# Performance work log

Measured on AMD Instinct MI355X. Metric: run time of the kernel, lower is better.

## Reference

```python
import jax, jax.numpy as jnp
import numpy as np

N_NODES = 50000
N_EDGES = 1_600_000
D_IN = 512
D_OUT = 512


def setup_inputs() -> dict:
    key = jax.random.key(0)
    k_x, k_w, k_b, k_r, k_c, k_e = jax.random.split(key, 6)
    x = jax.random.normal(k_x, (N_NODES, D_IN), dtype=jnp.float32)
    stdv = 1.0 / np.sqrt(D_OUT)
    weight = jax.random.uniform(k_w, (D_IN, D_OUT), minval=-stdv, maxval=stdv, dtype=jnp.float32)
    bias = jax.random.uniform(k_b, (D_OUT,), minval=-stdv, maxval=stdv, dtype=jnp.float32)
    row = jax.random.randint(k_r, (N_EDGES,), 0, N_NODES, dtype=jnp.int32)
    col = jax.random.randint(k_c, (N_EDGES,), 0, N_NODES, dtype=jnp.int32)
    edge_weight = jax.random.uniform(k_e, (N_EDGES,), dtype=jnp.float32)
    return {"x": x, "weight": weight, "bias": bias, "row": row, "col": col, "edge_weight": edge_weight}


def reference(x, weight, bias, row, col, edge_weight):
    # support = X @ W   [N, D_OUT]
    support = x @ weight
    # spmm: out[i] = sum_{e: row[e]==i} edge_weight[e] * support[col[e]]
    msgs = edge_weight[:, None] * support[col]  # [E, D_OUT]
    out = jax.ops.segment_sum(msgs, row, num_segments=N_NODES)
    return out + bias
```

## Files before the change

### kernel.cpp

```cpp
#include <hip/hip_runtime.h>
#include <hip/hip_fp16.h>

#define D_DIM 512
#define BM 128
#define BN 256
#define BK 64

typedef _Float16 h8 __attribute__((ext_vector_type(8)));
typedef _Float16 h4 __attribute__((ext_vector_type(4)));
typedef float f32x4 __attribute__((ext_vector_type(4)));
typedef unsigned int u32x4 __attribute__((ext_vector_type(4)));

#define LDS_PTR(p) ((__attribute__((address_space(3))) void*)(p))
#define GLB_PTR(p) ((const __attribute__((address_space(1))) void*)(p))


__global__ void k_count(const int* __restrict__ row, int* __restrict__ counts, int E) {
    int e = blockIdx.x * blockDim.x + threadIdx.x;
    if (e < E) atomicAdd(&counts[row[e]], 1);
}

__global__ void k_scan_part(const int* __restrict__ counts, int* __restrict__ offsets,
                            int* __restrict__ bsum, int n) {
    __shared__ int s[1024];
    int t = threadIdx.x;
    int i = blockIdx.x * 1024 + t;
    int v = (i < n) ? counts[i] : 0;
    s[t] = v;
    __syncthreads();
    for (int off = 1; off < 1024; off <<= 1) {
        int x = (t >= off) ? s[t - off] : 0;
        __syncthreads();
        s[t] += x;
        __syncthreads();
    }
    if (i < n) offsets[i] = s[t] - v;
    if (t == 1023) bsum[blockIdx.x] = s[t];
}

__global__ void k_scan_top(int* __restrict__ bsum, int* __restrict__ offsets, int nb, int n) {
    int t = threadIdx.x;
    int v = (t < nb) ? bsum[t] : 0;
    int orig = v;
    for (int off = 1; off < 64; off <<= 1) {
        int u = __shfl_up(v, off, 64);
        if (t >= off) v += u;
    }
    if (t < nb) bsum[t] = v - orig;
    if (t == nb - 1) offsets[n] = v;
}

__global__ void k_scan_add(int* __restrict__ offsets, int* __restrict__ cursor,
                           const int* __restrict__ bsum, int n) {
    int i = blockIdx.x * 1024 + threadIdx.x;
    if (i < n) {
        int o = offsets[i] + bsum[blockIdx.x];
        offsets[i] = o;
        cursor[i] = o;
    }
}

__global__ void k_scatter(const int* __restrict__ row, const int* __restrict__ col,
                          const float* __restrict__ ew, int* __restrict__ cursor,
                          uint2* __restrict__ packed, int E) {
    int e = blockIdx.x * blockDim.x + threadIdx.x;
    if (e < E) {
        int r = row[e];
        int pos = atomicAdd(&cursor[r], 1);
        packed[pos] = make_uint2((unsigned)col[e], __float_as_uint(ew[e]));
    }
}


__global__ void k_wt(const float* __restrict__ w, _Float16* __restrict__ wt) {
    __shared__ _Float16 tile[32][33];
    int bx = blockIdx.x & 15, by = blockIdx.x >> 4;
    int tx = threadIdx.x & 31, ty = threadIdx.x >> 5;
    for (int r = 0; r < 32; r += 8)
        tile[ty + r][tx] = (_Float16)w[(size_t)(by * 32 + ty + r) * 512 + bx * 32 + tx];
    __syncthreads();
    for (int r = 0; r < 32; r += 8)
        wt[(size_t)(bx * 32 + ty + r) * 512 + by * 32 + tx] = tile[tx][ty + r];
}


__launch_bounds__(256)
__global__ void k_gemm(const float* __restrict__ x, const _Float16* __restrict__ wt,
                       _Float16* __restrict__ sup, int M, int nwg) {
    __shared__ __align__(16) unsigned char As[BM * BK * 2];
    __shared__ __align__(16) unsigned char Bs[BN * BK * 2];

    const int orig = blockIdx.x;
    const int q = nwg >> 3, r = nwg & 7;
    const int xcd = orig & 7, idx = orig >> 3;
    const int wgid = (xcd < r ? xcd * (q + 1) : r * (q + 1) + (xcd - r) * q) + idx;
    const int m0 = (wgid >> 1) * BM, n0 = (wgid & 1) * BN;

    const int t = threadIdx.x;
    const int lane = t & 63, w = t >> 6;

    f32x4 acc[8][4] = {};

    const int ar_t = t >> 4;
    const int ac_t = (t & 15) * 4;
    const int bn_t = t >> 3;
    const int bk_sw = ((t & 7) * 16) ^ (((t >> 3) & 7) << 4);

    for (int kt = 0; kt < D_DIM / BK; ++kt) {
        const int k0 = kt * BK;
        for (int j = 0; j < 8; ++j) {
            int n = j * 32 + bn_t;
            const char* src = (const char*)(wt + (size_t)(n0 + n) * 512 + k0) + bk_sw;
            __builtin_amdgcn_global_load_lds(GLB_PTR(src), LDS_PTR(Bs + j * 4096 + t * 16),
                                             16, 0, 0);
        }
        for (int i = 0; i < 8; ++i) {
            int rr = i * 16 + ar_t;
            int g = m0 + rr;
            if (g >= M) g = M - 1;
            const float4 v = *(const float4*)(x + (size_t)g * 512 + k0 + ac_t);
            h4 hv;
            hv[0] = (_Float16)v.x; hv[1] = (_Float16)v.y;
            hv[2] = (_Float16)v.z; hv[3] = (_Float16)v.w;
            int addr = rr * 128 + ((ac_t * 2) ^ ((rr & 7) << 4));
            *(h4*)(As + addr) = hv;
        }
        __syncthreads();

        for (int ks = 0; ks < 2; ++ks) {
            h8 af[8], bf[4];
            const int kb = ks * 64 + ((lane >> 4) * 16);
#pragma unroll
            for (int mb = 0; mb < 8; ++mb) {
                int rr = mb * 16 + (lane & 15);
                af[mb] = *(const h8*)(As + rr * 128 + (kb ^ ((rr & 7) << 4)));
            }
#pragma unroll
            for (int nb = 0; nb < 4; ++nb) {
                int n = w * 64 + nb * 16 + (lane & 15);
                bf[nb] = *(const h8*)(Bs + n * 128 + (kb ^ ((n & 7) << 4)));
            }
#pragma unroll
            for (int mb = 0; mb < 8; ++mb)
#pragma unroll
                for (int nb = 0; nb < 4; ++nb)
                    acc[mb][nb] = __builtin_amdgcn_mfma_f32_16x16x32_f16(
                        af[mb], bf[nb], acc[mb][nb], 0, 0, 0);
        }
        __syncthreads();
    }

    const int cr = (lane >> 4) * 4, cc = lane & 15;
#pragma unroll
    for (int mb = 0; mb < 8; ++mb) {
#pragma unroll
        for (int nb = 0; nb < 4; ++nb) {
            int gn = n0 + w * 64 + nb * 16 + cc;
#pragma unroll
            for (int qq = 0; qq < 4; ++qq) {
                int gm = m0 + mb * 16 + cr + qq;
                if (gm < M)
                    sup[(size_t)gm * 512 + gn] = (_Float16)acc[mb][nb][qq];
            }
        }
    }
}


__global__ void k_spmm(const _Float16* __restrict__ sup, const uint2* __restrict__ packed,
                       const int* __restrict__ offsets, const float* __restrict__ bias,
                       float* __restrict__ out, int M) {
    const int i = blockIdx.x * 4 + (threadIdx.x >> 6);
    if (i >= M) return;
    const int l = threadIdx.x & 63;
    const int s0 = offsets[i], s1 = offsets[i + 1];
    const _Float16* __restrict__ supl = sup + l * 8;

    float acc[8];
    {
        const float4 b0 = *(const float4*)(bias + l * 8);
        const float4 b1 = *(const float4*)(bias + l * 8 + 4);
        acc[0] = b0.x; acc[1] = b0.y; acc[2] = b0.z; acc[3] = b0.w;
        acc[4] = b1.x; acc[5] = b1.y; acc[6] = b1.z; acc[7] = b1.w;
    }

    int e = s0;
    if ((e & 1) && e < s1) {
        uint2 p = packed[e];
        float wgt = __uint_as_float(p.y);
        h8 h = *(const h8*)(supl + (size_t)p.x * 512);
#pragma unroll
        for (int j = 0; j < 8; ++j) acc[j] += wgt * (float)h[j];
        ++e;
    }
    for (; e + 8 <= s1; e += 8) {
        const u32x4 q0 = __builtin_nontemporal_load((const u32x4*)(packed + e));
        const u32x4 q1 = __builtin_nontemporal_load((const u32x4*)(packed + e + 2));
        const u32x4 q2 = __builtin_nontemporal_load((const u32x4*)(packed + e + 4));
        const u32x4 q3 = __builtin_nontemporal_load((const u32x4*)(packed + e + 6));
        const h8 h0 = *(const h8*)(supl + (size_t)q0[0] * 512);
        const h8 h1 = *(const h8*)(supl + (size_t)q0[2] * 512);
        const h8 h2 = *(const h8*)(supl + (size_t)q1[0] * 512);
        const h8 h3 = *(const h8*)(supl + (size_t)q1[2] * 512);
        const h8 h4v = *(const h8*)(supl + (size_t)q2[0] * 512);
        const h8 h5 = *(const h8*)(supl + (size_t)q2[2] * 512);
        const h8 h6 = *(const h8*)(supl + (size_t)q3[0] * 512);
        const h8 h7 = *(const h8*)(supl + (size_t)q3[2] * 512);
        const float w0 = __uint_as_float(q0[1]), w1 = __uint_as_float(q0[3]);
        const float w2 = __uint_as_float(q1[1]), w3 = __uint_as_float(q1[3]);
        const float w4 = __uint_as_float(q2[1]), w5 = __uint_as_float(q2[3]);
        const float w6 = __uint_as_float(q3[1]), w7 = __uint_as_float(q3[3]);
#pragma unroll
        for (int j = 0; j < 8; ++j) {
            float a = acc[j];
            a += w0 * (float)h0[j];
            a += w1 * (float)h1[j];
            a += w2 * (float)h2[j];
            a += w3 * (float)h3[j];
            a += w4 * (float)h4v[j];
            a += w5 * (float)h5[j];
            a += w6 * (float)h6[j];
            a += w7 * (float)h7[j];
            acc[j] = a;
        }
    }
    for (; e < s1; ++e) {
        uint2 p = packed[e];
        float wgt = __uint_as_float(p.y);
        h8 h = *(const h8*)(supl + (size_t)p.x * 512);
#pragma unroll
        for (int j = 0; j < 8; ++j) acc[j] += wgt * (float)h[j];
    }

    f32x4 o0 = {acc[0], acc[1], acc[2], acc[3]};
    f32x4 o1 = {acc[4], acc[5], acc[6], acc[7]};
    __builtin_nontemporal_store(o0, (f32x4*)(out + (size_t)i * 512 + l * 8));
    __builtin_nontemporal_store(o1, (f32x4*)(out + (size_t)i * 512 + l * 8 + 4));
}


extern "C" void kernel_launch(void* const* d_in, const int* in_sizes, int n_in,
                              void* d_out, int out_size, void* d_ws, size_t ws_size,
                              hipStream_t stream) {
    const float* x      = (const float*)d_in[0];
    const float* weight = (const float*)d_in[1];
    const float* bias   = (const float*)d_in[2];
    const int*   row    = (const int*)d_in[3];
    const int*   col    = (const int*)d_in[4];
    const float* ew     = (const float*)d_in[5];
    const int M = in_sizes[0] / D_DIM;
    const int E = in_sizes[3];
    float* out = (float*)d_out;

    char* ws = (char*)d_ws;
    size_t off = 0;
    auto alloc = [&](size_t bytes) {
        void* p = ws + off;
        off = (off + bytes + 255) & ~(size_t)255;
        return p;
    };
    _Float16* sup  = (_Float16*)alloc((size_t)M * D_DIM * 2);
    _Float16* wt   = (_Float16*)alloc((size_t)512 * 512 * 2);
    int* counts    = (int*)alloc((size_t)M * 4);
    int* offsets   = (int*)alloc((size_t)(M + 1) * 4);
    int* cursor    = (int*)alloc((size_t)M * 4);
    int* bsum      = (int*)alloc(64 * 4);
    uint2* packed  = (uint2*)alloc((size_t)E * 8);
    (void)ws_size; (void)n_in; (void)out_size;

    (void)hipMemsetAsync(counts, 0, (size_t)M * 4, stream);
    k_count<<<(E + 255) / 256, 256, 0, stream>>>(row, counts, E);
    const int SB = (M + 1023) / 1024;
    k_scan_part<<<SB, 1024, 0, stream>>>(counts, offsets, bsum, M);
    k_scan_top<<<1, 64, 0, stream>>>(bsum, offsets, SB, M);
    k_scan_add<<<SB, 1024, 0, stream>>>(offsets, cursor, bsum, M);
    k_scatter<<<(E + 255) / 256, 256, 0, stream>>>(row, col, ew, cursor, packed, E);

    k_wt<<<256, 256, 0, stream>>>(weight, wt);
    const int nwg = ((M + BM - 1) / BM) * (D_DIM / BN);
    k_gemm<<<nwg, 256, 0, stream>>>(x, wt, sup, M, nwg);

    k_spmm<<<(M + 3) / 4, 256, 0, stream>>>(sup, packed, offsets, bias, out, M);
}
```

Before: 655.6 us.

## Split SpMM feature dimension into four column quarters across blocks

The SpMM kernel now launches four blocks per group of four rows. Each block handles a 128-column quarter, and each lane loads two halves (4 bytes) per edge instead of eight (16 bytes). This gives four times more waves, which should help hide gather latency for random column indices. In exchange, every edge's packed index/weight pair is re-read four times, the gathers become narrow 4-byte accesses, and the nontemporal loads and stores are replaced with ordinary ones.

```diff
diff --git a/kernel.cpp b/kernel.cpp
--- a/kernel.cpp
+++ b/kernel.cpp
@@ -8,6 +8,7 @@
 
 typedef _Float16 h8 __attribute__((ext_vector_type(8)));
 typedef _Float16 h4 __attribute__((ext_vector_type(4)));
+typedef _Float16 h2 __attribute__((ext_vector_type(2)));
 typedef float f32x4 __attribute__((ext_vector_type(4)));
 typedef unsigned int u32x4 __attribute__((ext_vector_type(4)));
 
@@ -170,72 +171,58 @@
 __global__ void k_spmm(const _Float16* __restrict__ sup, const uint2* __restrict__ packed,
                        const int* __restrict__ offsets, const float* __restrict__ bias,
                        float* __restrict__ out, int M) {
-    const int i = blockIdx.x * 4 + (threadIdx.x >> 6);
+    const int b = blockIdx.x;
+    const int qd = b & 3;
+    const int i = (b >> 2) * 4 + (threadIdx.x >> 6);
     if (i >= M) return;
     const int l = threadIdx.x & 63;
+    const int dcol = qd * 128 + l * 2;
+    const _Float16* __restrict__ supl = sup + dcol;
     const int s0 = offsets[i], s1 = offsets[i + 1];
-    const _Float16* __restrict__ supl = sup + l * 8;
-
-    float acc[8];
-    {
-        const float4 b0 = *(const float4*)(bias + l * 8);
-        const float4 b1 = *(const float4*)(bias + l * 8 + 4);
-        acc[0] = b0.x; acc[1] = b0.y; acc[2] = b0.z; acc[3] = b0.w;
-        acc[4] = b1.x; acc[5] = b1.y; acc[6] = b1.z; acc[7] = b1.w;
-    }
+
+    const float2 bb = *(const float2*)(bias + dcol);
+    float a0 = bb.x, a1 = bb.y;
 
     int e = s0;
     if ((e & 1) && e < s1) {
         uint2 p = packed[e];
         float wgt = __uint_as_float(p.y);
-        h8 h = *(const h8*)(supl + (size_t)p.x * 512);
-#pragma unroll
-        for (int j = 0; j < 8; ++j) acc[j] += wgt * (float)h[j];
+        h2 h = *(const h2*)(supl + (size_t)p.x * 512);
+        a0 += wgt * (float)h[0];
+        a1 += wgt * (float)h[1];
         ++e;
     }
     for (; e + 8 <= s1; e += 8) {
-        const u32x4 q0 = __builtin_nontemporal_load((const u32x4*)(packed + e));
-        const u32x4 q1 = __builtin_nontemporal_load((const u32x4*)(packed + e + 2));
-        const u32x4 q2 = __builtin_nontemporal_load((const u32x4*)(packed + e + 4));
-        const u32x4 q3 = __builtin_nontemporal_load((const u32x4*)(packed + e + 6));
-        const h8 h0 = *(const h8*)(supl + (size_t)q0[0] * 512);
-        const h8 h1 = *(const h8*)(supl + (size_t)q0[2] * 512);
-        const h8 h2 = *(const h8*)(supl + (size_t)q1[0] * 512);
-        const h8 h3 = *(const h8*)(supl + (size_t)q1[2] * 512);
-        const h8 h4v = *(const h8*)(supl + (size_t)q2[0] * 512);
-        const h8 h5 = *(const h8*)(supl + (size_t)q2[2] * 512);
-        const h8 h6 = *(const h8*)(supl + (size_t)q3[0] * 512);
-        const h8 h7 = *(const h8*)(supl + (size_t)q3[2] * 512);
+        const u32x4 q0 = *(const u32x4*)(packed + e);
+        const u32x4 q1 = *(const u32x4*)(packed + e + 2);
+        const u32x4 q2 = *(const u32x4*)(packed + e + 4);
+        const u32x4 q3 = *(const u32x4*)(packed + e + 6);
+        const h2 h0 = *(const h2*)(supl + (size_t)q0[0] * 512);
+        const h2 h1 = *(const h2*)(supl + (size_t)q0[2] * 512);
+        const h2 h2v = *(const h2*)(supl + (size_t)q1[0] * 512);
+        const h2 h3 = *(const h2*)(supl + (size_t)q1[2] * 512);
+        const h2 h4v = *(const h2*)(supl + (size_t)q2[0] * 512);
+        const h2 h5 = *(const h2*)(supl + (size_t)q2[2] * 512);
+        const h2 h6 = *(const h2*)(supl + (size_t)q3[0] * 512);
+        const h2 h7 = *(const h2*)(supl + (size_t)q3[2] * 512);
         const float w0 = __uint_as_float(q0[1]), w1 = __uint_as_float(q0[3]);
         const float w2 = __uint_as_float(q1[1]), w3 = __uint_as_float(q1[3]);
         const float w4 = __uint_as_float(q2[1]), w5 = __uint_as_float(q2[3]);
         const float w6 = __uint_as_float(q3[1]), w7 = __uint_as_float(q3[3]);
-#pragma unroll
-        for (int j = 0; j < 8; ++j) {
-            float a = acc[j];
-            a += w0 * (float)h0[j];
-            a += w1 * (float)h1[j];
-            a += w2 * (float)h2[j];
-            a += w3 * (float)h3[j];
-            a += w4 * (float)h4v[j];
-            a += w5 * (float)h5[j];
-            a += w6 * (float)h6[j];
-            a += w7 * (float)h7[j];
-            acc[j] = a;
-        }
+        a0 += w0 * (float)h0[0] + w1 * (float)h1[0] + w2 * (float)h2v[0] + w3 * (float)h3[0]
+            + w4 * (float)h4v[0] + w5 * (float)h5[0] + w6 * (float)h6[0] + w7 * (float)h7[0];
+        a1 += w0 * (float)h0[1] + w1 * (float)h1[1] + w2 * (float)h2v[1] + w3 * (float)h3[1]
+            + w4 * (float)h4v[1] + w5 * (float)h5[1] + w6 * (float)h6[1] + w7 * (float)h7[1];
     }
     for (; e < s1; ++e) {
         uint2 p = packed[e];
         float wgt = __uint_as_float(p.y);
-        h8 h = *(const h8*)(supl + (size_t)p.x * 512);
-#pragma unroll
-        for (int j = 0; j < 8; ++j) acc[j] += wgt * (float)h[j];
-    }
-
-    f32x4 o0 = {acc[0], acc[1], acc[2], acc[3]};
-    f32x4 o1 = {acc[4], acc[5], acc[6], acc[7]};
-    __builtin_nontemporal_store(o0, (f32x4*)(out + (size_t)i * 512 + l * 8));
-    __builtin_nontemporal_store(o1, (f32x4*)(out + (size_t)i * 512 + l * 8 + 4));
+        h2 h = *(const h2*)(supl + (size_t)p.x * 512);
+        a0 += wgt * (float)h[0];
+        a1 += wgt * (float)h[1];
+    }
+
+    *(float2*)(out + (size_t)i * 512 + dcol) = make_float2(a0, a1);
 }
 
 
@@ -280,5 +267,6 @@
     const int nwg = ((M + BM - 1) / BM) * (D_DIM / BN);
     k_gemm<<<nwg, 256, 0, stream>>>(x, wt, sup, M, nwg);
 
-    k_spmm<<<(M + 3) / 4, 256, 0, stream>>>(sup, packed, offsets, bias, out, M);
-}
+    const int rowgroups = (M + 3) / 4;
+    k_spmm<<<rowgroups * 4, 256, 0, stream>>>(sup, packed, offsets, bias, out, M);
+}
```

New measurement: 638.5 us. 1.03x faster.
